# Performance work log

Hardware: AMD Instinct MI355X
Metric: run time of the kernel (lower is better)

Reference implementation:

```python
import jax, jax.numpy as jnp
import numpy as np

IN_F, OUT_F, K, STRIDE, PAD = 256, 256, 3, 1, 1
SEARCH_SPACE = (2, 4, 8, 16)  # derived in __init__ from in/out=256, feature_size=16


def _cir_project(weight, b):
    """Circulant projection of conv weight for block size b.
    Equivalent to the nested diagonal-mean + roll loops in trans_to_cir:
      tc[q,p,i] = mean_j tmp[q,p,j,(j+i)%b]   (wrapped diagonal mean)
      w[q,p,r,c] = tc[q,p,(r-c)%b]            (roll construction)
    """
    q, p = OUT_F // b, IN_F // b
    tmp = weight.reshape(q, b, p, b, K, K).transpose(0, 2, 1, 3, 4, 5)  # (q,p,b,b,k,k)
    j = jnp.arange(b)
    diag_idx = (j[:, None] + j[None, :]) % b          # (b_j, b_i)
    tc = tmp[:, :, j[:, None], diag_idx].mean(axis=2)  # (q,p,b,k,k)
    circ_idx = (j[:, None] - j[None, :]) % b          # (r, c)
    w = tc[:, :, circ_idx]                             # (q,p,b,b,k,k)
    return w.transpose(0, 2, 1, 3, 4, 5).reshape(OUT_F, IN_F, K, K)


def setup_inputs() -> dict:
    key = jax.random.key(0)
    k1, k2 = jax.random.split(key, 2)
    x = jax.random.normal(k1, (256, IN_F, 16, 16), jnp.float32)
    weight = jax.random.normal(k2, (OUT_F, IN_F, K, K), jnp.float32) * 0.05
    alphas = jnp.ones((len(SEARCH_SPACE) + 1,), jnp.float32)
    return {"x": x, "weight": weight, "alphas": alphas}


def reference(x, weight, alphas):
    # gumbel_softmax with finetune=False -> plain softmax over alphas
    a = jax.nn.softmax(alphas)
    w = a[0] * weight
    for i, b in enumerate(SEARCH_SPACE):
        w = w + a[i + 1] * _cir_project(weight, b)
    return jax.lax.conv_general_dilated(
        x, w,
        window_strides=(STRIDE, STRIDE),
        padding=[(PAD, PAD), (PAD, PAD)],
        dimension_numbers=("NCHW", "OIHW", "NCHW"),
    )
```

## Files before the change

kernel.cpp:

```cpp
#include <hip/hip_runtime.h>
#include <cstdint>
#include <cstddef>

#define NIMG 256
#define PADW 18
#define XB_IMG (PADW * PADW * 256)
#define W2_ROW 2304

typedef __bf16 bf16x8 __attribute__((ext_vector_type(8)));
typedef float floatx4 __attribute__((ext_vector_type(4)));
typedef float floatvec4 __attribute__((ext_vector_type(4)));

__device__ __forceinline__ unsigned short f2bf(float f) {
    unsigned u = __float_as_uint(f);
    u = (u + 0x7FFFu + ((u >> 16) & 1u)) >> 16;
    return (unsigned short)u;
}

__device__ __forceinline__ void gload_lds16(const void* g, void* l) {
    __builtin_amdgcn_global_load_lds(
        (const __attribute__((address_space(1))) void*)g,
        (__attribute__((address_space(3))) void*)l, 16, 0, 0);
}

#define VMCNT_LGKM0(n) asm volatile("s_waitcnt vmcnt(" #n ") lgkmcnt(0)" ::: "memory")

__global__ __launch_bounds__(256) void prep_kernel(
        const float* __restrict__ x, unsigned short* __restrict__ xb,
        const float* __restrict__ wt, const float* __restrict__ alphas,
        unsigned short* __restrict__ w2) {
    __shared__ __align__(16) char lds_pool[64 * 268 * 2];
    const int bx = blockIdx.x;
    const int t  = threadIdx.x;

    if (bx < 1024) {
        unsigned short (*tile2)[268] = (unsigned short (*)[268])lds_pool;
        const int n  = bx & 255;
        const int cy = bx >> 8;
        const int c0 = cy * 64;
        const float* xi = x + (size_t)n * 65536;
        unsigned short* xo = xb + (size_t)n * XB_IMG;

        if (cy == 0) {
            #pragma unroll
            for (int it = 0; it < 17; ++it) {
                int idx = it * 256 + t;
                int hp = idx >> 6;
                int c4 = (idx & 63) * 4;
                int py, px;
                if (hp < 18)      { py = 0;       px = hp;      }
                else if (hp < 36) { py = 17;      px = hp - 18; }
                else if (hp < 52) { py = hp - 35; px = 0;       }
                else              { py = hp - 51; px = 17;      }
                *(uint2*)&xo[(py * 18 + px) * 256 + c4] = make_uint2(0u, 0u);
            }
        }
        {
            const int p4 = (t & 63) * 4;
            const int ci = t >> 6;
            #pragma unroll
            for (int i = 0; i < 16; ++i) {
                const int c = i * 4 + ci;
                floatvec4 v = *(const floatvec4*)&xi[(c0 + c) * 256 + p4];
                unsigned lo = (unsigned)f2bf(v.x) | ((unsigned)f2bf(v.y) << 16);
                unsigned hi = (unsigned)f2bf(v.z) | ((unsigned)f2bf(v.w) << 16);
                *(uint2*)&tile2[c][p4] = make_uint2(lo, hi);
            }
        }
        __syncthreads();
        #pragma unroll
        for (int it = 0; it < 32; ++it) {
            int idx = it * 256 + t;
            int p   = idx >> 5;
            int cp  = (idx & 31) * 2;
            unsigned lo = tile2[cp][p];
            unsigned hi = tile2[cp + 1][p];
            int py = (p >> 4) + 1, px = (p & 15) + 1;
            *(unsigned int*)&xo[(py * 18 + px) * 256 + c0 + cp] = lo | (hi << 16);
        }
    } else {
        float (*wlds)[257] = (float (*)[257])lds_pool;
        const int w   = bx - 1024;
        const int o16 = (w & 15) * 16;
        const int pos = w >> 4;

        #pragma unroll
        for (int j = 0; j < 16; ++j)
            wlds[j][t] = wt[((o16 + j) * 256 + t) * 9 + pos];

        float a[5];
        {
            float mx = alphas[0];
            #pragma unroll
            for (int i = 1; i < 5; ++i) mx = fmaxf(mx, alphas[i]);
            float s = 0.f;
            #pragma unroll
            for (int i = 0; i < 5; ++i) { a[i] = __expf(alphas[i] - mx); s += a[i]; }
            float inv = 1.f / s;
            #pragma unroll
            for (int i = 0; i < 5; ++i) a[i] *= inv;
        }
        __syncthreads();

        const int c = t;
        #pragma unroll
        for (int oo = 0; oo < 16; ++oo) {
            float acc = a[0] * wlds[oo][c];
            #pragma unroll
            for (int bi = 0; bi < 4; ++bi) {
                const int b  = 2 << bi;
                const int r  = oo & (b - 1);
                const int cc = c & (b - 1);
                const int i0 = (r - cc) & (b - 1);
                const int ob = oo - r;
                const int icb = c - cc;
                float s2 = 0.f;
                for (int j = 0; j < b; ++j)
                    s2 += wlds[ob + j][icb + ((j + i0) & (b - 1))];
                acc += a[1 + bi] * s2 * (1.f / (float)b);
            }
            w2[(size_t)(o16 + oo) * W2_ROW + pos * 256 + c] = f2bf(acc);
        }
    }
}

__global__ __launch_bounds__(256) void wprep_kernel(
        const float* __restrict__ wt, const float* __restrict__ alphas,
        unsigned short* __restrict__ w2) {
    __shared__ float wlds[16][257];
    const int o16 = blockIdx.x * 16;
    const int pos = blockIdx.y;
    const int t   = threadIdx.x;
    #pragma unroll
    for (int j = 0; j < 16; ++j)
        wlds[j][t] = wt[((o16 + j) * 256 + t) * 9 + pos];
    float a[5];
    {
        float mx = alphas[0];
        #pragma unroll
        for (int i = 1; i < 5; ++i) mx = fmaxf(mx, alphas[i]);
        float s = 0.f;
        #pragma unroll
        for (int i = 0; i < 5; ++i) { a[i] = __expf(alphas[i] - mx); s += a[i]; }
        float inv = 1.f / s;
        #pragma unroll
        for (int i = 0; i < 5; ++i) a[i] *= inv;
    }
    __syncthreads();
    const int c = t;
    #pragma unroll
    for (int oo = 0; oo < 16; ++oo) {
        float acc = a[0] * wlds[oo][c];
        #pragma unroll
        for (int bi = 0; bi < 4; ++bi) {
            const int b  = 2 << bi;
            const int r  = oo & (b - 1);
            const int cc = c & (b - 1);
            const int i0 = (r - cc) & (b - 1);
            const int ob = oo - r;
            const int icb = c - cc;
            float s2 = 0.f;
            for (int j = 0; j < b; ++j)
                s2 += wlds[ob + j][icb + ((j + i0) & (b - 1))];
            acc += a[1 + bi] * s2 * (1.f / (float)b);
        }
        w2[(size_t)(o16 + oo) * W2_ROW + pos * 256 + c] = f2bf(acc);
    }
}

__global__ __launch_bounds__(512, 2) void gemm_kernel(
        const unsigned short* __restrict__ xb,
        const unsigned short* __restrict__ w2,
        float* __restrict__ out) {
    extern __shared__ __align__(16) char smem[];
    unsigned short* const xs = (unsigned short*)smem;
    unsigned short* const ws = (unsigned short*)(smem + 65536);

    const int t     = threadIdx.x;
    const int lane  = t & 63;
    const int wid   = t >> 6;
    const int n_img = blockIdx.x;

    const int q     = lane >> 2;
    const int kswz  = ((lane & 3) - ((lane >> 3) & 3)) & 3;
    const int choff = kswz * 8;
    const unsigned short* sbase;
    int sg[4];
    int ldst;
    if (wid < 4) {
        sbase = xb;
        #pragma unroll
        for (int i = 0; i < 4; ++i) {
            const int r = wid * 64 + i * 16 + q;
            const int y = r >> 4, xx = r & 15;
            sg[i] = n_img * XB_IMG + ((y + 1) * 18 + (xx + 1)) * 256 + choff;
        }
        ldst = wid * 4096;
    } else {
        sbase = w2;
        const int wv = wid - 4;
        #pragma unroll
        for (int i = 0; i < 4; ++i) {
            const int r = wv * 64 + i * 16 + q;
            sg[i] = r * W2_ROW + choff;
        }
        ldst = (wid - 4) * 4096;
    }
    const bool is_x = (wid < 4);

    auto issue = [&](int hs, unsigned short* XSb, unsigned short* WSb) {
        const int pos = hs >> 3, k32 = hs & 7;
        int go; char* dst;
        if (is_x) {
            const int dy = pos / 3, dx = pos - dy * 3;
            go  = (dy - 1) * 4608 + (dx - 1) * 256 + k32 * 32;
            dst = (char*)XSb + ldst;
        } else {
            go  = pos * 256 + k32 * 32;
            dst = (char*)WSb + ldst;
        }
        #pragma unroll
        for (int i = 0; i < 4; ++i)
            gload_lds16(sbase + sg[i] + go, dst + i * 1024);
    };

    const int wr   = wid >> 2, wc = wid & 3;
    const int slot = ((lane >> 1) + (lane >> 4)) & 3;
    const int aoff = (wr * 128 + (lane & 15)) * 32 + slot * 8;
    const int boff = (wc * 64  + (lane & 15)) * 32 + slot * 8;

    const floatx4 z4 = {0.f, 0.f, 0.f, 0.f};
    floatx4 acc[8][4];
    #pragma unroll
    for (int i = 0; i < 8; ++i)
        #pragma unroll
        for (int j = 0; j < 4; ++j) acc[i][j] = z4;

    auto compute = [&](const unsigned short* XSb, const unsigned short* WSb) {
        bf16x8 af[8], bfr[4];
        #pragma unroll
        for (int mt = 0; mt < 8; ++mt)
            af[mt] = *(const bf16x8*)&WSb[aoff + mt * 512];
        #pragma unroll
        for (int nt = 0; nt < 4; ++nt)
            bfr[nt] = *(const bf16x8*)&XSb[boff + nt * 512];
        __builtin_amdgcn_s_setprio(1);
        #pragma unroll
        for (int mt = 0; mt < 8; ++mt)
            #pragma unroll
            for (int nt = 0; nt < 4; ++nt)
                acc[mt][nt] = __builtin_amdgcn_mfma_f32_16x16x32_bf16(
                    af[mt], bfr[nt], acc[mt][nt], 0, 0, 0);
        __builtin_amdgcn_s_setprio(0);
    };

    unsigned short* const xs0 = xs,         * const ws0 = ws;
    unsigned short* const xs1 = xs + 8192,  * const ws1 = ws + 8192;
    unsigned short* const xs2 = xs + 16384, * const ws2 = ws + 16384;
    unsigned short* const xs3 = xs + 24576, * const ws3 = ws + 24576;

    issue(0, xs0, ws0);
    issue(1, xs1, ws1);
    issue(2, xs2, ws2);

    int hs = 0;
    #pragma unroll 1
    for (int it = 0; it < 17; ++it) {
        VMCNT_LGKM0(8); __builtin_amdgcn_s_barrier();
        issue(hs + 3, xs3, ws3);
        compute(xs0, ws0);

        VMCNT_LGKM0(8); __builtin_amdgcn_s_barrier();
        issue(hs + 4, xs0, ws0);
        compute(xs1, ws1);

        VMCNT_LGKM0(8); __builtin_amdgcn_s_barrier();
        issue(hs + 5, xs1, ws1);
        compute(xs2, ws2);

        VMCNT_LGKM0(8); __builtin_amdgcn_s_barrier();
        issue(hs + 6, xs2, ws2);
        compute(xs3, ws3);
        hs += 4;
    }
    VMCNT_LGKM0(8); __builtin_amdgcn_s_barrier();
    issue(71, xs3, ws3);
    compute(xs0, ws0);

    VMCNT_LGKM0(8); __builtin_amdgcn_s_barrier();
    compute(xs1, ws1);

    VMCNT_LGKM0(4); __builtin_amdgcn_s_barrier();
    compute(xs2, ws2);

    VMCNT_LGKM0(0); __builtin_amdgcn_s_barrier();
    compute(xs3, ws3);

    float* ob = out + (size_t)n_img * 65536;
    const int kb = wr * 128 + (lane >> 4) * 4;
    const int pb = wc * 64 + (lane & 15);
    #pragma unroll
    for (int mt = 0; mt < 8; ++mt)
        #pragma unroll
        for (int nt = 0; nt < 4; ++nt) {
            const int kout = kb + mt * 16;
            const int p    = pb + nt * 16;
            #pragma unroll
            for (int r = 0; r < 4; ++r)
                ob[(size_t)(kout + r) * 256 + p] = acc[mt][nt][r];
        }
}

__global__ __launch_bounds__(256) void naive_conv(
        const float* __restrict__ x, const unsigned short* __restrict__ w2,
        float* __restrict__ out) {
    __shared__ float wr[2304];
    const int n = blockIdx.x >> 8, k = blockIdx.x & 255;
    const int t = threadIdx.x;
    for (int i = t; i < 2304; i += 256)
        wr[i] = __uint_as_float(((unsigned)w2[k * W2_ROW + i]) << 16);
    __syncthreads();
    const int y = t >> 4, xx = t & 15;
    const float* xi = x + (size_t)n * 65536;
    float acc = 0.f;
    for (int pos = 0; pos < 9; ++pos) {
        int dy = pos / 3 - 1, dx = pos % 3 - 1;
        int yy = y + dy, x2 = xx + dx;
        if (yy < 0 || yy > 15 || x2 < 0 || x2 > 15) continue;
        const float* xp = xi + yy * 16 + x2;
        const float* wp = wr + pos * 256;
        for (int c = 0; c < 256; ++c) acc += xp[c * 256] * wp[c];
    }
    out[(size_t)n * 65536 + k * 256 + t] = acc;
}

extern "C" void kernel_launch(void* const* d_in, const int* in_sizes, int n_in,
                              void* d_out, int out_size, void* d_ws, size_t ws_size,
                              hipStream_t stream) {
    const float* x      = (const float*)d_in[0];
    const float* wt     = (const float*)d_in[1];
    const float* alphas = (const float*)d_in[2];
    float* out = (float*)d_out;

    const size_t xb_elems = (size_t)NIMG * XB_IMG;
    const size_t w2_elems = (size_t)256 * W2_ROW;
    const size_t need = (xb_elems + w2_elems) * sizeof(unsigned short);

    if (ws_size >= need) {
        unsigned short* xbp = (unsigned short*)d_ws;
        unsigned short* w2p = xbp + xb_elems;
        static bool attr_done = false;
        if (!attr_done) {
            (void)hipFuncSetAttribute(reinterpret_cast<const void*>(&gemm_kernel),
                                      hipFuncAttributeMaxDynamicSharedMemorySize,
                                      131072);
            attr_done = true;
        }
        prep_kernel<<<dim3(1168), 256, 0, stream>>>(x, xbp, wt, alphas, w2p);
        gemm_kernel<<<dim3(256), 512, 131072, stream>>>(xbp, w2p, out);
    } else if (ws_size >= w2_elems * sizeof(unsigned short)) {
        unsigned short* w2p = (unsigned short*)d_ws;
        wprep_kernel<<<dim3(16, 9), 256, 0, stream>>>(wt, alphas, w2p);
        naive_conv<<<dim3(256 * 256), 256, 0, stream>>>(x, w2p, out);
    }
}
```

Measured before the change: 186.9 us.

## Split each k-step into two MFMA halves interleaved with LDS reads and global-to-LDS issues

Restructures the main loop so that each stage loads half of the A fragments, issues half of the next global-to-LDS copies, runs 16 MFMAs, then loads the other half and issues the rest before the next 16 MFMAs. Extra barriers and sched_barriers pin this ordering. The k-step decomposition also changes from position-major to channel-chunk-major (hs/9 vs hs&7), which alters the global access order. The aim is finer interleaving of memory and matrix work, at the cost of more barriers per stage. The reordered index mapping could also affect correctness or cache locality.

Result: no change. 188.1 us (+0.6%).

```diff
diff --git a/kernel.cpp b/kernel.cpp
--- a/kernel.cpp
+++ b/kernel.cpp
@@ -208,20 +208,19 @@
     }
     const bool is_x = (wid < 4);
 
-    auto issue = [&](int hs, unsigned short* XSb, unsigned short* WSb) {
-        const int pos = hs >> 3, k32 = hs & 7;
+    auto issue2 = [&](int hsp, char* px, char* pw, int i0) {
+        const int c32 = hsp / 9, pos = hsp - c32 * 9;
         int go; char* dst;
         if (is_x) {
-            const int dy = pos / 3, dx = pos - dy * 3;
-            go  = (dy - 1) * 4608 + (dx - 1) * 256 + k32 * 32;
-            dst = (char*)XSb + ldst;
+            const int dy = pos / 3, dxp = pos - dy * 3;
+            go  = (dy - 1) * 4608 + (dxp - 1) * 256 + c32 * 32;
+            dst = px + ldst;
         } else {
-            go  = pos * 256 + k32 * 32;
-            dst = (char*)WSb + ldst;
-        }
-        #pragma unroll
-        for (int i = 0; i < 4; ++i)
-            gload_lds16(sbase + sg[i] + go, dst + i * 1024);
+            go  = pos * 256 + c32 * 32;
+            dst = pw + ldst;
+        }
+        gload_lds16(sbase + sg[i0]     + go, dst + i0 * 1024);
+        gload_lds16(sbase + sg[i0 + 1] + go, dst + (i0 + 1) * 1024);
     };
 
     const int wr   = wid >> 2, wc = wid & 3;
@@ -236,65 +235,69 @@
         #pragma unroll
         for (int j = 0; j < 4; ++j) acc[i][j] = z4;
 
-    auto compute = [&](const unsigned short* XSb, const unsigned short* WSb) {
-        bf16x8 af[8], bfr[4];
-        #pragma unroll
-        for (int mt = 0; mt < 8; ++mt)
-            af[mt] = *(const bf16x8*)&WSb[aoff + mt * 512];
-        #pragma unroll
-        for (int nt = 0; nt < 4; ++nt)
-            bfr[nt] = *(const bf16x8*)&XSb[boff + nt * 512];
-        __builtin_amdgcn_s_setprio(1);
-        #pragma unroll
-        for (int mt = 0; mt < 8; ++mt)
-            #pragma unroll
-            for (int nt = 0; nt < 4; ++nt)
-                acc[mt][nt] = __builtin_amdgcn_mfma_f32_16x16x32_bf16(
-                    af[mt], bfr[nt], acc[mt][nt], 0, 0, 0);
-        __builtin_amdgcn_s_setprio(0);
-    };
-
     unsigned short* const xs0 = xs,         * const ws0 = ws;
     unsigned short* const xs1 = xs + 8192,  * const ws1 = ws + 8192;
     unsigned short* const xs2 = xs + 16384, * const ws2 = ws + 16384;
     unsigned short* const xs3 = xs + 24576, * const ws3 = ws + 24576;
 
-    issue(0, xs0, ws0);
-    issue(1, xs1, ws1);
-    issue(2, xs2, ws2);
+#define HALF(CX, CW, PX, PW, HSP, DOISS, N) do {                              \
+    VMCNT_LGKM0(N);                                                           \
+    __builtin_amdgcn_s_barrier();                                             \
+    bf16x8 afq[4], bq[4];                                                     \
+    _Pragma("unroll")                                                         \
+    for (int mt = 0; mt < 4; ++mt)                                            \
+        afq[mt] = *(const bf16x8*)&(CW)[aoff + mt * 512];                     \
+    _Pragma("unroll")                                                         \
+    for (int nt = 0; nt < 4; ++nt)                                            \
+        bq[nt] = *(const bf16x8*)&(CX)[boff + nt * 512];                      \
+    if (DOISS) issue2((HSP), (char*)(PX), (char*)(PW), 0);                    \
+    __builtin_amdgcn_s_barrier();                                             \
+    asm volatile("s_waitcnt lgkmcnt(0)" ::: "memory");                        \
+    __builtin_amdgcn_sched_barrier(0);                                        \
+    __builtin_amdgcn_s_setprio(1);                                            \
+    _Pragma("unroll")                                                         \
+    for (int mt = 0; mt < 4; ++mt)                                            \
+        _Pragma("unroll")                                                     \
+        for (int nt = 0; nt < 4; ++nt)                                        \
+            acc[mt][nt] = __builtin_amdgcn_mfma_f32_16x16x32_bf16(            \
+                afq[mt], bq[nt], acc[mt][nt], 0, 0, 0);                       \
+    __builtin_amdgcn_s_setprio(0);                                            \
+    bf16x8 agq[4];                                                            \
+    _Pragma("unroll")                                                         \
+    for (int mt = 0; mt < 4; ++mt)                                            \
+        agq[mt] = *(const bf16x8*)&(CW)[aoff + (mt + 4) * 512];               \
+    if (DOISS) issue2((HSP), (char*)(PX), (char*)(PW), 2);                    \
+    __builtin_amdgcn_s_barrier();                                             \
+    asm volatile("s_waitcnt lgkmcnt(0)" ::: "memory");                        \
+    __builtin_amdgcn_sched_barrier(0);                                        \
+    __builtin_amdgcn_s_setprio(1);                                            \
+    _Pragma("unroll")                                                         \
+    for (int mt = 0; mt < 4; ++mt)                                            \
+        _Pragma("unroll")                                                     \
+        for (int nt = 0; nt < 4; ++nt)                                        \
+            acc[mt + 4][nt] = __builtin_amdgcn_mfma_f32_16x16x32_bf16(        \
+                agq[mt], bq[nt], acc[mt + 4][nt], 0, 0, 0);                   \
+    __builtin_amdgcn_s_setprio(0);                                            \
+} while (0)
+
+    issue2(0, (char*)xs0, (char*)ws0, 0); issue2(0, (char*)xs0, (char*)ws0, 2);
+    issue2(1, (char*)xs1, (char*)ws1, 0); issue2(1, (char*)xs1, (char*)ws1, 2);
+    issue2(2, (char*)xs2, (char*)ws2, 0); issue2(2, (char*)xs2, (char*)ws2, 2);
 
     int hs = 0;
     #pragma unroll 1
     for (int it = 0; it < 17; ++it) {
-        VMCNT_LGKM0(8); __builtin_amdgcn_s_barrier();
-        issue(hs + 3, xs3, ws3);
-        compute(xs0, ws0);
-
-        VMCNT_LGKM0(8); __builtin_amdgcn_s_barrier();
-        issue(hs + 4, xs0, ws0);
-        compute(xs1, ws1);
-
-        VMCNT_LGKM0(8); __builtin_amdgcn_s_barrier();
-        issue(hs + 5, xs1, ws1);
-        compute(xs2, ws2);
-
-        VMCNT_LGKM0(8); __builtin_amdgcn_s_barrier();
-        issue(hs + 6, xs2, ws2);
-        compute(xs3, ws3);
+        HALF(xs0, ws0, xs3, ws3, hs + 3, true, 8);
+        HALF(xs1, ws1, xs0, ws0, hs + 4, true, 8);
+        HALF(xs2, ws2, xs1, ws1, hs + 5, true, 8);
+        HALF(xs3, ws3, xs2, ws2, hs + 6, true, 8);
         hs += 4;
     }
-    VMCNT_LGKM0(8); __builtin_amdgcn_s_barrier();
-    issue(71, xs3, ws3);
-    compute(xs0, ws0);
-
-    VMCNT_LGKM0(8); __builtin_amdgcn_s_barrier();
-    compute(xs1, ws1);
-
-    VMCNT_LGKM0(4); __builtin_amdgcn_s_barrier();
-    compute(xs2, ws2);
-
-    VMCNT_LGKM0(0); __builtin_amdgcn_s_barrier();
-    compute(xs3, ws3);
+    HALF(xs0, ws0, xs3, ws3, 71, true,  8);
+    HALF(xs1, ws1, xs0, ws0, 0,  false, 8);
+    HALF(xs2, ws2, xs0, ws0, 0,  false, 4);
+    HALF(xs3, ws3, xs0, ws0, 0,  false, 0);
+#undef HALF
 
     float* ob = out + (size_t)n_img * 65536;
     const int kb = wr * 128 + (lane >> 4) * 4;
```

## Stage channel-slab halo tiles in LDS and reuse them across the 3x3 taps

Applied to the files above, without the earlier changes.

The padded bf16 input is rewritten into 8 channel slabs of 32 channels, with a swizzle on the 16-byte chunks within each row. The GEMM now loads each half-image slab (rows plus halo) into LDS once per 32-channel chunk and reads all 9 filter taps from it by shifting the row index, instead of reloading the input tile for every tap. The grid is split into two blocks per image of 256 threads each, with static LDS and double buffering handled by __syncthreads in place of the 4-stage vmcnt pipeline. This cuts global and L2 traffic for activations, at the cost of a shallower pipeline and a barrier on every step.

Result: no change. 184.6 us (-1.2%).

```diff
diff --git a/kernel.cpp b/kernel.cpp
--- a/kernel.cpp
+++ b/kernel.cpp
@@ -5,6 +5,7 @@
 #define NIMG 256
 #define PADW 18
 #define XB_IMG (PADW * PADW * 256)
+#define SLAB_ELEMS (324 * 32)
 #define W2_ROW 2304
 
 typedef __bf16 bf16x8 __attribute__((ext_vector_type(8)));
@@ -22,8 +23,6 @@
         (const __attribute__((address_space(1))) void*)g,
         (__attribute__((address_space(3))) void*)l, 16, 0, 0);
 }
-
-#define VMCNT_LGKM0(n) asm volatile("s_waitcnt vmcnt(" #n ") lgkmcnt(0)" ::: "memory")
 
 __global__ __launch_bounds__(256) void prep_kernel(
         const float* __restrict__ x, unsigned short* __restrict__ xb,
@@ -42,17 +41,23 @@
         unsigned short* xo = xb + (size_t)n * XB_IMG;
 
         if (cy == 0) {
-            #pragma unroll
-            for (int it = 0; it < 17; ++it) {
-                int idx = it * 256 + t;
-                int hp = idx >> 6;
-                int c4 = (idx & 63) * 4;
+            if (t < 68) {
+                int hp = t;
                 int py, px;
                 if (hp < 18)      { py = 0;       px = hp;      }
                 else if (hp < 36) { py = 17;      px = hp - 18; }
                 else if (hp < 52) { py = hp - 35; px = 0;       }
                 else              { py = hp - 51; px = 17;      }
-                *(uint2*)&xo[(py * 18 + px) * 256 + c4] = make_uint2(0u, 0u);
+                const int r = py * 18 + px;
+                const uint4 z = make_uint4(0u, 0u, 0u, 0u);
+                #pragma unroll
+                for (int sl = 0; sl < 8; ++sl) {
+                    unsigned short* base = xo + sl * SLAB_ELEMS + r * 32;
+                    *(uint4*)&base[0]  = z;
+                    *(uint4*)&base[8]  = z;
+                    *(uint4*)&base[16] = z;
+                    *(uint4*)&base[24] = z;
+                }
             }
         }
         {
@@ -69,14 +74,20 @@
         }
         __syncthreads();
         #pragma unroll
-        for (int it = 0; it < 32; ++it) {
-            int idx = it * 256 + t;
-            int p   = idx >> 5;
-            int cp  = (idx & 31) * 2;
-            unsigned lo = tile2[cp][p];
-            unsigned hi = tile2[cp + 1][p];
-            int py = (p >> 4) + 1, px = (p & 15) + 1;
-            *(unsigned int*)&xo[(py * 18 + px) * 256 + c0 + cp] = lo | (hi << 16);
+        for (int it = 0; it < 8; ++it) {
+            const int U  = it * 256 + t;
+            const int u  = U & 3;
+            const int qq = (U >> 2) & 1;
+            const int p  = U >> 3;
+            const int r  = ((p >> 4) + 1) * 18 + (p & 15) + 1;
+            const int ks = (u - ((r >> 1) & 3)) & 3;
+            const int cb = qq * 32 + ks * 8;
+            unsigned v0 = (unsigned)tile2[cb + 0][p] | ((unsigned)tile2[cb + 1][p] << 16);
+            unsigned v1 = (unsigned)tile2[cb + 2][p] | ((unsigned)tile2[cb + 3][p] << 16);
+            unsigned v2 = (unsigned)tile2[cb + 4][p] | ((unsigned)tile2[cb + 5][p] << 16);
+            unsigned v3 = (unsigned)tile2[cb + 6][p] | ((unsigned)tile2[cb + 7][p] << 16);
+            const int sl = cy * 2 + qq;
+            *(uint4*)&xo[sl * SLAB_ELEMS + r * 32 + u * 8] = make_uint4(v0, v1, v2, v3);
         }
     } else {
         float (*wlds)[257] = (float (*)[257])lds_pool;
@@ -168,66 +179,44 @@
     }
 }
 
-__global__ __launch_bounds__(512, 2) void gemm_kernel(
+__global__ __launch_bounds__(256, 2) void gemm_kernel(
         const unsigned short* __restrict__ xb,
         const unsigned short* __restrict__ w2,
         float* __restrict__ out) {
-    extern __shared__ __align__(16) char smem[];
-    unsigned short* const xs = (unsigned short*)smem;
-    unsigned short* const ws = (unsigned short*)(smem + 65536);
-
-    const int t     = threadIdx.x;
-    const int lane  = t & 63;
-    const int wid   = t >> 6;
-    const int n_img = blockIdx.x;
+    __shared__ __align__(16) unsigned short as0[8192];
+    __shared__ __align__(16) unsigned short as1[8192];
+    __shared__ __align__(16) unsigned short sl0[6144];
+    __shared__ __align__(16) unsigned short sl1[6144];
+
+    const int t    = threadIdx.x;
+    const int lane = t & 63;
+    const int wid  = t >> 6;
+    const int bidx = blockIdx.x;
+    const int n_img = bidx >> 1;
+    const int half  = bidx & 1;
 
     const int q     = lane >> 2;
     const int kswz  = ((lane & 3) - ((lane >> 3) & 3)) & 3;
     const int choff = kswz * 8;
-    const unsigned short* sbase;
-    int sg[4];
-    int ldst;
-    if (wid < 4) {
-        sbase = xb;
-        #pragma unroll
-        for (int i = 0; i < 4; ++i) {
-            const int r = wid * 64 + i * 16 + q;
-            const int y = r >> 4, xx = r & 15;
-            sg[i] = n_img * XB_IMG + ((y + 1) * 18 + (xx + 1)) * 256 + choff;
-        }
-        ldst = wid * 4096;
-    } else {
-        sbase = w2;
-        const int wv = wid - 4;
-        #pragma unroll
-        for (int i = 0; i < 4; ++i) {
-            const int r = wv * 64 + i * 16 + q;
-            sg[i] = r * W2_ROW + choff;
-        }
-        ldst = (wid - 4) * 4096;
-    }
-    const bool is_x = (wid < 4);
-
-    auto issue = [&](int hs, unsigned short* XSb, unsigned short* WSb) {
-        const int pos = hs >> 3, k32 = hs & 7;
-        int go; char* dst;
-        if (is_x) {
-            const int dy = pos / 3, dx = pos - dy * 3;
-            go  = (dy - 1) * 4608 + (dx - 1) * 256 + k32 * 32;
-            dst = (char*)XSb + ldst;
-        } else {
-            go  = pos * 256 + k32 * 32;
-            dst = (char*)WSb + ldst;
-        }
-        #pragma unroll
-        for (int i = 0; i < 4; ++i)
-            gload_lds16(sbase + sg[i] + go, dst + i * 1024);
-    };
-
-    const int wr   = wid >> 2, wc = wid & 3;
-    const int slot = ((lane >> 1) + (lane >> 4)) & 3;
-    const int aoff = (wr * 128 + (lane & 15)) * 32 + slot * 8;
-    const int boff = (wc * 64  + (lane & 15)) * 32 + slot * 8;
+    int ag[4];
+    #pragma unroll
+    for (int i = 0; i < 4; ++i) {
+        const int r = wid * 64 + i * 16 + q;
+        ag[i] = r * W2_ROW + choff;
+    }
+    const int adst = wid * 4096;
+
+    const size_t slab_base = (size_t)n_img * XB_IMG + (size_t)half * 4608;
+    const int sll = lane * 8;
+
+    const int wr = wid >> 1, wc = wid & 1;
+    const int aslot = ((lane >> 1) + (lane >> 4)) & 3;
+    const int aoff  = (wr * 128 + (lane & 15)) * 32 + aslot * 8;
+    const int g4    = lane >> 4;
+    int rbase[4];
+    #pragma unroll
+    for (int nt = 0; nt < 4; ++nt)
+        rbase[nt] = (wc * 4 + nt) * 18 + (lane & 15);
 
     const floatx4 z4 = {0.f, 0.f, 0.f, 0.f};
     floatx4 acc[8][4];
@@ -236,69 +225,70 @@
         #pragma unroll
         for (int j = 0; j < 4; ++j) acc[i][j] = z4;
 
-    auto compute = [&](const unsigned short* XSb, const unsigned short* WSb) {
-        bf16x8 af[8], bfr[4];
+    #pragma unroll
+    for (int i = 0; i < 4; ++i)
+        gload_lds16(w2 + ag[i], (char*)as0 + adst + i * 1024);
+    #pragma unroll
+    for (int j = 0; j < 3; ++j) {
+        const int gg = wid * 3 + j;
+        gload_lds16(xb + slab_base + gg * 512 + sll, (char*)sl0 + gg * 1024);
+    }
+
+    int pos = 0, c32 = 0, sh = 0;
+    #pragma unroll 1
+    for (int s = 0; s < 72; ++s) {
+        __syncthreads();
+
+        if (s < 71) {
+            int posn = pos + 1, c32n = c32;
+            if (posn == 9) { posn = 0; ++c32n; }
+            const int go = posn * 256 + c32n * 32;
+            char* dstA = (s & 1) ? (char*)as0 : (char*)as1;
+            #pragma unroll
+            for (int i = 0; i < 4; ++i)
+                gload_lds16(w2 + ag[i] + go, dstA + adst + i * 1024);
+        }
+        if (pos == 7 && c32 < 7) {
+            const size_t src = slab_base + (size_t)(c32 + 1) * SLAB_ELEMS;
+            char* dstS = (c32 & 1) ? (char*)sl0 : (char*)sl1;
+            #pragma unroll
+            for (int j = 0; j < 3; ++j) {
+                const int gg = wid * 3 + j;
+                gload_lds16(xb + src + gg * 512 + sll, dstS + gg * 1024);
+            }
+        }
+
+        const unsigned short* AS = (s & 1) ? as1 : as0;
+        const unsigned short* SL = (c32 & 1) ? sl1 : sl0;
+
+        bf16x8 af[8], bq[4];
         #pragma unroll
         for (int mt = 0; mt < 8; ++mt)
-            af[mt] = *(const bf16x8*)&WSb[aoff + mt * 512];
-        #pragma unroll
-        for (int nt = 0; nt < 4; ++nt)
-            bfr[nt] = *(const bf16x8*)&XSb[boff + nt * 512];
+            af[mt] = *(const bf16x8*)&AS[aoff + mt * 512];
+        #pragma unroll
+        for (int nt = 0; nt < 4; ++nt) {
+            const int rl = rbase[nt] + sh;
+            const int bo = rl * 32 + ((((rl >> 1) + g4) & 3) << 3);
+            bq[nt] = *(const bf16x8*)&SL[bo];
+        }
+
         __builtin_amdgcn_s_setprio(1);
         #pragma unroll
         for (int mt = 0; mt < 8; ++mt)
             #pragma unroll
             for (int nt = 0; nt < 4; ++nt)
                 acc[mt][nt] = __builtin_amdgcn_mfma_f32_16x16x32_bf16(
-                    af[mt], bfr[nt], acc[mt][nt], 0, 0, 0);
+                    af[mt], bq[nt], acc[mt][nt], 0, 0, 0);
         __builtin_amdgcn_s_setprio(0);
-    };
-
-    unsigned short* const xs0 = xs,         * const ws0 = ws;
-    unsigned short* const xs1 = xs + 8192,  * const ws1 = ws + 8192;
-    unsigned short* const xs2 = xs + 16384, * const ws2 = ws + 16384;
-    unsigned short* const xs3 = xs + 24576, * const ws3 = ws + 24576;
-
-    issue(0, xs0, ws0);
-    issue(1, xs1, ws1);
-    issue(2, xs2, ws2);
-
-    int hs = 0;
-    #pragma unroll 1
-    for (int it = 0; it < 17; ++it) {
-        VMCNT_LGKM0(8); __builtin_amdgcn_s_barrier();
-        issue(hs + 3, xs3, ws3);
-        compute(xs0, ws0);
-
-        VMCNT_LGKM0(8); __builtin_amdgcn_s_barrier();
-        issue(hs + 4, xs0, ws0);
-        compute(xs1, ws1);
-
-        VMCNT_LGKM0(8); __builtin_amdgcn_s_barrier();
-        issue(hs + 5, xs1, ws1);
-        compute(xs2, ws2);
-
-        VMCNT_LGKM0(8); __builtin_amdgcn_s_barrier();
-        issue(hs + 6, xs2, ws2);
-        compute(xs3, ws3);
-        hs += 4;
-    }
-    VMCNT_LGKM0(8); __builtin_amdgcn_s_barrier();
-    issue(71, xs3, ws3);
-    compute(xs0, ws0);
-
-    VMCNT_LGKM0(8); __builtin_amdgcn_s_barrier();
-    compute(xs1, ws1);
-
-    VMCNT_LGKM0(4); __builtin_amdgcn_s_barrier();
-    compute(xs2, ws2);
-
-    VMCNT_LGKM0(0); __builtin_amdgcn_s_barrier();
-    compute(xs3, ws3);
+
+        ++pos; ++sh;
+        if (pos == 3 || pos == 6) sh += 15;
+        if (pos == 9) { pos = 0; sh = 0; ++c32; }
+    }
 
     float* ob = out + (size_t)n_img * 65536;
     const int kb = wr * 128 + (lane >> 4) * 4;
-    const int pb = wc * 64 + (lane & 15);
+    const int pb = half * 128 + wc * 64 + (lane & 15);
     #pragma unroll
     for (int mt = 0; mt < 8; ++mt)
         #pragma unroll
@@ -349,15 +339,8 @@
     if (ws_size >= need) {
         unsigned short* xbp = (unsigned short*)d_ws;
         unsigned short* w2p = xbp + xb_elems;
-        static bool attr_done = false;
-        if (!attr_done) {
-            (void)hipFuncSetAttribute(reinterpret_cast<const void*>(&gemm_kernel),
-                                      hipFuncAttributeMaxDynamicSharedMemorySize,
-                                      131072);
-            attr_done = true;
-        }
         prep_kernel<<<dim3(1168), 256, 0, stream>>>(x, xbp, wt, alphas, w2p);
-        gemm_kernel<<<dim3(256), 512, 131072, stream>>>(xbp, w2p, out);
+        gemm_kernel<<<dim3(512), 256, 0, stream>>>(xbp, w2p, out);
     } else if (ws_size >= w2_elems * sizeof(unsigned short)) {
         unsigned short* w2p = (unsigned short*)d_ws;
         wprep_kernel<<<dim3(16, 9), 256, 0, stream>>>(wt, alphas, w2p);
```
